# Kernel optimization log

Measured on AMD Instinct MI355X. Metric: run time of the kernel, lower is better.

Reference implementation:

```python
import jax, jax.numpy as jnp
import numpy as np

NUM_HEADS = 32
NUM_KV_HEADS = 8
HEAD_DIM = 128
HIDDEN = 4096
RANK = 8
ALPHA = 16.0
SCALING = ALPHA / RANK
EPS = 1e-8


def dora_linear(x, W, A, B, m):
    # DoRA: W_eff = W + scaling * B @ A; directional component normalized per
    # output row, rescaled by learned magnitude m.
    W_eff = W + SCALING * (B @ A)                      # [out, in]
    norm = jnp.linalg.norm(W_eff, axis=1)              # [out]
    W_d = W_eff * (m / (norm + EPS))[:, None]
    return x @ W_d.T


def setup_inputs() -> dict:
    key = jax.random.key(0)
    ks = jax.random.split(key, 16)
    B_, S = 2, 2048
    hidden_states = jax.random.normal(ks[0], (B_, S, HIDDEN), jnp.float32)
    # additive causal mask
    causal = jnp.triu(jnp.full((S, S), -1e9, jnp.float32), k=1)
    attention_mask = jnp.broadcast_to(causal, (B_, 1, S, S))

    def w(k, shape, scale=0.02):
        return scale * jax.random.normal(k, shape, jnp.float32)

    Wq = w(ks[1], (HIDDEN, HIDDEN)); Aq = w(ks[2], (RANK, HIDDEN)); Bq = w(ks[3], (HIDDEN, RANK))
    Wk = w(ks[4], (NUM_KV_HEADS * HEAD_DIM, HIDDEN)); Ak = w(ks[5], (RANK, HIDDEN)); Bk = w(ks[6], (NUM_KV_HEADS * HEAD_DIM, RANK))
    Wv = w(ks[7], (NUM_KV_HEADS * HEAD_DIM, HIDDEN)); Av = w(ks[8], (RANK, HIDDEN)); Bv = w(ks[9], (NUM_KV_HEADS * HEAD_DIM, RANK))
    Wo = w(ks[10], (HIDDEN, HIDDEN)); Ao = w(ks[11], (RANK, HIDDEN)); Bo = w(ks[12], (HIDDEN, RANK))
    # DoRA magnitude init: column-norm of base weight (per output row)
    mq = jnp.linalg.norm(Wq, axis=1)
    mk = jnp.linalg.norm(Wk, axis=1)
    mv = jnp.linalg.norm(Wv, axis=1)
    mo = jnp.linalg.norm(Wo, axis=1)
    return dict(hidden_states=hidden_states, attention_mask=attention_mask,
                Wq=Wq, Aq=Aq, Bq=Bq, mq=mq,
                Wk=Wk, Ak=Ak, Bk=Bk, mk=mk,
                Wv=Wv, Av=Av, Bv=Bv, mv=mv,
                Wo=Wo, Ao=Ao, Bo=Bo, mo=mo)


def reference(hidden_states, attention_mask,
              Wq, Aq, Bq, mq, Wk, Ak, Bk, mk,
              Wv, Av, Bv, mv, Wo, Ao, Bo, mo):
    bsz, q_len, _ = hidden_states.shape
    n_rep = NUM_HEADS // NUM_KV_HEADS

    q = dora_linear(hidden_states, Wq, Aq, Bq, mq)
    k = dora_linear(hidden_states, Wk, Ak, Bk, mk)
    v = dora_linear(hidden_states, Wv, Av, Bv, mv)

    q = q.reshape(bsz, q_len, NUM_HEADS, HEAD_DIM).transpose(0, 2, 1, 3)
    k = k.reshape(bsz, q_len, NUM_KV_HEADS, HEAD_DIM).transpose(0, 2, 1, 3)
    v = v.reshape(bsz, q_len, NUM_KV_HEADS, HEAD_DIM).transpose(0, 2, 1, 3)

    # _apply_rotary_pos_emb is a no-op in the source: (q, k) unchanged

    # repeat_kv for grouped-query attention
    k = jnp.repeat(k, n_rep, axis=1)  # [b, H, s, d]
    v = jnp.repeat(v, n_rep, axis=1)

    scale = 1.0 / jnp.sqrt(jnp.float32(HEAD_DIM))
    attn_weights = jnp.einsum('bhqd,bhkd->bhqk', q, k) * scale
    attn_weights = attn_weights + attention_mask
    attn_weights = jax.nn.softmax(attn_weights, axis=-1)
    attn_output = jnp.einsum('bhqk,bhkd->bhqd', attn_weights, v)
    attn_output = attn_output.transpose(0, 2, 1, 3).reshape(bsz, q_len, HIDDEN)
    attn_output = dora_linear(attn_output, Wo, Ao, Bo, mo)
    return attn_output
```

## Files before the change

kernel.cpp:

```cpp
#include <hip/hip_runtime.h>
#include <hip/hip_bf16.h>
#include <stdint.h>

#define HIDDEN 4096
#define RANK   8
#define SCALING 2.0f
#define EPS    1e-8f
#define SEQ    2048
#define BATCH  2
#define NH     32
#define NKVH   8
#define HD     128
#define MROWS  (BATCH*SEQ)
#define NQKV   6144

typedef __attribute__((ext_vector_type(8))) short bf16x8;
typedef __attribute__((ext_vector_type(4))) short bf16x4;
typedef __attribute__((ext_vector_type(4))) float f32x4;

__device__ __forceinline__ void gload_lds16(const void* g, void* lds) {
  __builtin_amdgcn_global_load_lds((__attribute__((address_space(1))) void*)g,
                                   (__attribute__((address_space(3))) void*)lds,
                                   16, 0, 0);
}

__device__ __forceinline__ unsigned short f2bf(float f) {
  __hip_bfloat16 h = __float2bfloat16(f);
  return *reinterpret_cast<unsigned short*>(&h);
}

__device__ __forceinline__ void store_c(float* p, float v) { *p = v; }
__device__ __forceinline__ void store_c(__hip_bfloat16* p, float v) { *p = __float2bfloat16(v); }

__device__ __forceinline__ bf16x8 lds_read8_b64(const short* p) {
  bf16x4 lo = *(const bf16x4*)p;
  bf16x4 hi = *(const bf16x4*)(p + 4);
  bf16x8 r;
  r[0]=lo[0]; r[1]=lo[1]; r[2]=lo[2]; r[3]=lo[3];
  r[4]=hi[0]; r[5]=hi[1]; r[6]=hi[2]; r[7]=hi[3];
  return r;
}

__device__ __forceinline__ void wd_row(const float* __restrict__ W, const float* __restrict__ A,
                                       const float* __restrict__ B, const float* __restrict__ m,
                                       unsigned short* __restrict__ out, int row, int tid,
                                       float* wsum) {
  float bl[RANK];
#pragma unroll
  for (int t = 0; t < RANK; ++t) bl[t] = SCALING * B[row*RANK + t];
  float ev[16];
  float ss = 0.f;
#pragma unroll
  for (int it = 0; it < 4; ++it) {
    const int j = it*1024 + tid*4;
    const float4 wv = *(const float4*)&W[(size_t)row*HIDDEN + j];
    float e0 = wv.x, e1 = wv.y, e2 = wv.z, e3 = wv.w;
#pragma unroll
    for (int t = 0; t < RANK; ++t) {
      const float4 av = *(const float4*)&A[t*HIDDEN + j];
      e0 += bl[t]*av.x; e1 += bl[t]*av.y; e2 += bl[t]*av.z; e3 += bl[t]*av.w;
    }
    ev[it*4+0]=e0; ev[it*4+1]=e1; ev[it*4+2]=e2; ev[it*4+3]=e3;
    ss += e0*e0 + e1*e1 + e2*e2 + e3*e3;
  }
#pragma unroll
  for (int off = 32; off > 0; off >>= 1) ss += __shfl_down(ss, off, 64);
  if ((tid & 63) == 0) wsum[tid >> 6] = ss;
  __syncthreads();
  const float norm = sqrtf(wsum[0]+wsum[1]+wsum[2]+wsum[3]);
  const float scl = m[row] / (norm + EPS);
#pragma unroll
  for (int it = 0; it < 4; ++it) {
    const int j = it*1024 + tid*4;
    ushort4 pk;
    pk.x = f2bf(ev[it*4+0]*scl); pk.y = f2bf(ev[it*4+1]*scl);
    pk.z = f2bf(ev[it*4+2]*scl); pk.w = f2bf(ev[it*4+3]*scl);
    *(ushort4*)&out[(size_t)row*HIDDEN + j] = pk;
  }
}

__launch_bounds__(256)
__global__ void prep_kernel(const float* __restrict__ x, unsigned short* __restrict__ xbf,
                            const float* Wq, const float* Aq, const float* Bq, const float* mq, unsigned short* wdq,
                            const float* Wk, const float* Ak, const float* Bk, const float* mk, unsigned short* wdk,
                            const float* Wv, const float* Av, const float* Bv, const float* mv, unsigned short* wdv,
                            const float* Wo, const float* Ao, const float* Bo, const float* mo, unsigned short* wdo) {
  __shared__ float wsum[4];
  const int bid = blockIdx.x;
  const int tid = threadIdx.x;
  if (bid < 16384) {
    const size_t i = ((size_t)bid * 256 + tid) * 4;
    const float4 v = *(const float4*)&x[i];
    ushort4 pk;
    pk.x = f2bf(v.x); pk.y = f2bf(v.y); pk.z = f2bf(v.z); pk.w = f2bf(v.w);
    *(ushort4*)&xbf[i] = pk;
  } else if (bid < 20480) {
    wd_row(Wq, Aq, Bq, mq, wdq, bid - 16384, tid, wsum);
  } else if (bid < 21504) {
    wd_row(Wk, Ak, Bk, mk, wdk, bid - 20480, tid, wsum);
  } else if (bid < 22528) {
    wd_row(Wv, Av, Bv, mv, wdv, bid - 21504, tid, wsum);
  } else {
    wd_row(Wo, Ao, Bo, mo, wdo, bid - 22528, tid, wsum);
  }
}

__launch_bounds__(256)
__global__ void wd_kernel(const float* __restrict__ W, const float* __restrict__ A,
                          const float* __restrict__ B, const float* __restrict__ m,
                          unsigned short* __restrict__ out) {
  __shared__ float wsum[4];
  wd_row(W, A, B, m, out, blockIdx.x, threadIdx.x, wsum);
}

template<typename CT>
__launch_bounds__(256)
__global__ void gemm_bt(const __hip_bfloat16* __restrict__ A,
                        const __hip_bfloat16* __restrict__ B,
                        CT* __restrict__ C, const int M, const int N, const int K) {
  __shared__ __hip_bfloat16 As[128*64];
  __shared__ __hip_bfloat16 Bs[128*64];
  const int tid = threadIdx.x;
  const int w = tid >> 6, l = tid & 63;
  const int tM = blockIdx.y * 128, tN = blockIdx.x * 128;
  const int wm = (w >> 1) * 64, wn = (w & 1) * 64;
  const int lr = l >> 3;
  const int lcs = ((l & 7) ^ lr) * 8;
  const int q4 = l >> 4;
  const int ln = l & 15;
  const int sw = ln & 7;
  f32x4 acc[4][4] = {};
  const __hip_bfloat16* Ab = A + (size_t)tM * K;
  const __hip_bfloat16* Bb = B + (size_t)tN * K;
  for (int k0 = 0; k0 < K; k0 += 64) {
    __syncthreads();
#pragma unroll
    for (int i = 0; i < 4; ++i) {
      const int rr = i*32 + w*8;
      gload_lds16(Ab + (size_t)(rr + lr)*K + (k0 + lcs), &As[rr*64]);
      gload_lds16(Bb + (size_t)(rr + lr)*K + (k0 + lcs), &Bs[rr*64]);
    }
    __syncthreads();
    const short* Ap = (const short*)As;
    const short* Bp = (const short*)Bs;
#pragma unroll
    for (int ks = 0; ks < 2; ++ks) {
      const int slot = ((ks*4 + q4) ^ sw) * 8;
      bf16x8 af[4], bff[4];
#pragma unroll
      for (int mi = 0; mi < 4; ++mi)
        af[mi] = *(const bf16x8*)&Ap[(wm + mi*16 + ln)*64 + slot];
#pragma unroll
      for (int ni = 0; ni < 4; ++ni)
        bff[ni] = *(const bf16x8*)&Bp[(wn + ni*16 + ln)*64 + slot];
#pragma unroll
      for (int mi = 0; mi < 4; ++mi)
#pragma unroll
        for (int ni = 0; ni < 4; ++ni)
          acc[mi][ni] = __builtin_amdgcn_mfma_f32_16x16x32_bf16(af[mi], bff[ni], acc[mi][ni], 0, 0, 0);
    }
  }
  const int r0 = tM + wm + q4*4;
  const int c0 = tN + wn + ln;
#pragma unroll
  for (int mi = 0; mi < 4; ++mi)
#pragma unroll
    for (int ni = 0; ni < 4; ++ni)
#pragma unroll
      for (int r = 0; r < 4; ++r)
        store_c(&C[(size_t)(r0 + mi*16 + r)*N + c0 + ni*16], acc[mi][ni][r]);
}

#define VT_S 68
#define PS_S 68
__launch_bounds__(256, 3)
__global__ void attn_kernel(const __hip_bfloat16* __restrict__ qkv,
                            __hip_bfloat16* __restrict__ out) {
  const int bid = blockIdx.x;
  const int qt = 15 - (bid >> 6);
  const int hb = bid & 63;
  const int h  = hb & 31;
  const int b  = hb >> 5;
  const int kvh = h >> 2;
  const int tid = threadIdx.x;
  const int w = tid >> 6, l = tid & 63;
  const int q4 = l >> 4;
  const int ln = l & 15;
  const int sw = ln & 7;

  __shared__ __hip_bfloat16 Ks[64*128];
  __shared__ __hip_bfloat16 Vt[128*VT_S];
  __shared__ __hip_bfloat16 Ps[4][2][16*PS_S];

  const __hip_bfloat16* kb = qkv + (size_t)(b*SEQ)*NQKV + HIDDEN + kvh*HD;
  const __hip_bfloat16* vb = qkv + (size_t)(b*SEQ)*NQKV + (HIDDEN+1024) + kvh*HD;

  const int Q0 = qt*128;

  const int krow = l >> 4;
  const int kchunk = ((l & 15) ^ krow ^ ((w & 1) << 2)) * 8;

  const int vc4 = (tid & 15) * 4;
  const int vd0 = (tid >> 4) * 8;

  bf16x8 aq[2][4];
#pragma unroll
  for (int hf = 0; hf < 2; ++hf) {
    const __hip_bfloat16* qr = qkv + (size_t)(b*SEQ + Q0 + hf*64 + w*16 + ln)*NQKV + h*HD;
#pragma unroll
    for (int ks = 0; ks < 4; ++ks) {
      uint4 raw = *(const uint4*)(qr + ks*32 + q4*8);
      aq[hf][ks] = *(const bf16x8*)&raw;
    }
  }

  f32x4 o[2][8] = {};
  float mx[2] = {-1e30f, -1e30f};
  float lsum[2] = {0.f, 0.f};
  const float sc = 0.08838834764831845f;
  const int qabs0 = Q0 + w*16 + ln;

  const int jmax = 2*qt + 1;
  for (int j = 0; j <= jmax; ++j) {
    const int do0 = (j <= 2*qt);
    __syncthreads();
#pragma unroll
    for (int i = 0; i < 4; ++i) {
      const int rr = i*16 + w*4;
      gload_lds16(kb + (size_t)(j*64 + rr + krow)*NQKV + kchunk, &Ks[rr*128]);
    }
    {
      uint4 r0 = *(const uint4*)(vb + (size_t)(j*64 + vc4 + 0)*NQKV + vd0);
      uint4 r1 = *(const uint4*)(vb + (size_t)(j*64 + vc4 + 1)*NQKV + vd0);
      uint4 r2 = *(const uint4*)(vb + (size_t)(j*64 + vc4 + 2)*NQKV + vd0);
      uint4 r3 = *(const uint4*)(vb + (size_t)(j*64 + vc4 + 3)*NQKV + vd0);
      const unsigned short* p0 = (const unsigned short*)&r0;
      const unsigned short* p1 = (const unsigned short*)&r1;
      const unsigned short* p2 = (const unsigned short*)&r2;
      const unsigned short* p3 = (const unsigned short*)&r3;
#pragma unroll
      for (int t = 0; t < 8; ++t) {
        ushort4 pk; pk.x = p0[t]; pk.y = p1[t]; pk.z = p2[t]; pk.w = p3[t];
        *(ushort4*)&Vt[(vd0 + t)*VT_S + vc4] = pk;
      }
    }
    __syncthreads();

    f32x4 s[2][4] = {};
    const short* Kp = (const short*)Ks;
#pragma unroll
    for (int ks = 0; ks < 4; ++ks) {
      const int slot = ((ks*4 + q4) ^ sw) * 8;
#pragma unroll
      for (int nt = 0; nt < 4; ++nt) {
        bf16x8 bk = *(const bf16x8*)&Kp[(nt*16 + ln)*128 + slot];
        if (do0) s[0][nt] = __builtin_amdgcn_mfma_f32_16x16x32_bf16(bk, aq[0][ks], s[0][nt], 0, 0, 0);
        s[1][nt] = __builtin_amdgcn_mfma_f32_16x16x32_bf16(bk, aq[1][ks], s[1][nt], 0, 0, 0);
      }
    }

#pragma unroll
    for (int hf = 0; hf < 2; ++hf) {
      if (hf == 0 && !do0) continue;
      const int qabs = qabs0 + hf*64;
      if (j == 2*qt + hf) {
#pragma unroll
        for (int nt = 0; nt < 4; ++nt)
#pragma unroll
          for (int r = 0; r < 4; ++r) {
            const int kvabs = j*64 + nt*16 + q4*4 + r;
            if (kvabs > qabs) s[hf][nt][r] = -1e30f;
          }
      }
      float vmax = mx[hf];
#pragma unroll
      for (int nt = 0; nt < 4; ++nt)
#pragma unroll
        for (int r = 0; r < 4; ++r) vmax = fmaxf(vmax, s[hf][nt][r]);
      vmax = fmaxf(vmax, __shfl_xor(vmax, 16, 64));
      vmax = fmaxf(vmax, __shfl_xor(vmax, 32, 64));
      const float alpha = __expf((mx[hf] - vmax) * sc);
      float rs = 0.f;
#pragma unroll
      for (int nt = 0; nt < 4; ++nt)
#pragma unroll
        for (int r = 0; r < 4; ++r) {
          const float e = __expf((s[hf][nt][r] - vmax) * sc);
          s[hf][nt][r] = e; rs += e;
        }
      rs += __shfl_xor(rs, 16, 64);
      rs += __shfl_xor(rs, 32, 64);
      mx[hf] = vmax;
      lsum[hf] = lsum[hf]*alpha + rs;
#pragma unroll
      for (int r = 0; r < 4; ++r) {
        const float ar = __shfl(alpha, q4*4 + r, 64);
#pragma unroll
        for (int ni = 0; ni < 8; ++ni) o[hf][ni][r] *= ar;
      }
      __hip_bfloat16* Pw = Ps[w][hf];
#pragma unroll
      for (int nt = 0; nt < 4; ++nt) {
        ushort4 pk;
        pk.x = f2bf(s[hf][nt][0]); pk.y = f2bf(s[hf][nt][1]);
        pk.z = f2bf(s[hf][nt][2]); pk.w = f2bf(s[hf][nt][3]);
        *(ushort4*)&Pw[ln*PS_S + nt*16 + q4*4] = pk;
      }
    }

    const short* Vp = (const short*)Vt;
    const short* Pp0 = (const short*)Ps[w][0];
    const short* Pp1 = (const short*)Ps[w][1];
#pragma unroll
    for (int ks = 0; ks < 2; ++ks) {
      bf16x8 ap0 = lds_read8_b64(&Pp0[ln*PS_S + ks*32 + q4*8]);
      bf16x8 ap1 = lds_read8_b64(&Pp1[ln*PS_S + ks*32 + q4*8]);
#pragma unroll
      for (int ni = 0; ni < 8; ++ni) {
        bf16x8 bv = lds_read8_b64(&Vp[(ni*16 + ln)*VT_S + ks*32 + q4*8]);
        if (do0) o[0][ni] = __builtin_amdgcn_mfma_f32_16x16x32_bf16(ap0, bv, o[0][ni], 0, 0, 0);
        o[1][ni] = __builtin_amdgcn_mfma_f32_16x16x32_bf16(ap1, bv, o[1][ni], 0, 0, 0);
      }
    }
  }

#pragma unroll
  for (int hf = 0; hf < 2; ++hf) {
    const int row0 = b*SEQ + Q0 + hf*64 + w*16 + q4*4;
#pragma unroll
    for (int r = 0; r < 4; ++r) {
      const float lr = __shfl(lsum[hf], q4*4 + r, 64);
      const float inv = 1.f / lr;
#pragma unroll
      for (int ni = 0; ni < 8; ++ni)
        out[(size_t)(row0 + r)*HIDDEN + h*HD + ni*16 + ln] = __float2bfloat16(o[hf][ni][r] * inv);
    }
  }
}

extern "C" void kernel_launch(void* const* d_in, const int* in_sizes, int n_in,
                              void* d_out, int out_size, void* d_ws, size_t ws_size,
                              hipStream_t stream) {
  (void)in_sizes; (void)n_in; (void)out_size;
  const float* x  = (const float*)d_in[0];
  const float* Wq = (const float*)d_in[2];
  const float* Aq = (const float*)d_in[3];
  const float* Bq = (const float*)d_in[4];
  const float* mq = (const float*)d_in[5];
  const float* Wk = (const float*)d_in[6];
  const float* Ak = (const float*)d_in[7];
  const float* Bk = (const float*)d_in[8];
  const float* mk = (const float*)d_in[9];
  const float* Wv = (const float*)d_in[10];
  const float* Av = (const float*)d_in[11];
  const float* Bv = (const float*)d_in[12];
  const float* mv = (const float*)d_in[13];
  const float* Wo = (const float*)d_in[14];
  const float* Ao = (const float*)d_in[15];
  const float* Bo = (const float*)d_in[16];
  const float* mo = (const float*)d_in[17];

  char* ws = (char*)d_ws;
  __hip_bfloat16* xbf = (__hip_bfloat16*)ws;
  __hip_bfloat16* wd  = (__hip_bfloat16*)(ws + (size_t)33554432);
  __hip_bfloat16* qkv = (__hip_bfloat16*)(ws + (size_t)83886080);
  const bool big = ws_size >= (size_t)167772160;
  __hip_bfloat16* wdo = big ? (__hip_bfloat16*)(ws + (size_t)134217728) : wd;

  prep_kernel<<<big ? 26624 : 22528, 256, 0, stream>>>(
      x, (unsigned short*)xbf,
      Wq, Aq, Bq, mq, (unsigned short*)wd,
      Wk, Ak, Bk, mk, (unsigned short*)(wd + (size_t)4096*4096),
      Wv, Av, Bv, mv, (unsigned short*)(wd + (size_t)5120*4096),
      Wo, Ao, Bo, mo, (unsigned short*)wdo);
  gemm_bt<__hip_bfloat16><<<dim3(48, 32), 256, 0, stream>>>(xbf, wd, qkv, MROWS, NQKV, HIDDEN);
  if (!big)
    wd_kernel<<<4096, 256, 0, stream>>>(Wo, Ao, Bo, mo, (unsigned short*)wdo);
  attn_kernel<<<1024, 256, 0, stream>>>(qkv, xbf);
  gemm_bt<float><<<dim3(32, 32), 256, 0, stream>>>(xbf, wdo, (float*)d_out, MROWS, HIDDEN, HIDDEN);
}
```

Baseline: 825.7 us.

## Replace GEMM with 256x256-tile double-buffered pipelined kernel and XCD-aware block mapping

Replaces the 128x128 single-buffered bf16 GEMM with a 512-thread kernel computing 256x256 tiles. The K loop is split into quarter-stages that issue the next stage's global-to-LDS loads while the current stage's MFMAs run, using a double-buffered 128KB LDS region, explicit vmcnt waits and s_setprio around the MFMA bursts. Block IDs are remapped so neighbouring tiles land on the same XCD for L2 reuse. The aim is to hide load latency and raise arithmetic intensity in both projection GEMMs. The cost is a heavier LDS and register footprint with lower occupancy, and correctness depends on the hand-placed barrier and waitcnt ordering.

```diff
diff --git a/kernel.cpp b/kernel.cpp
--- a/kernel.cpp
+++ b/kernel.cpp
@@ -113,62 +113,99 @@
   wd_row(W, A, B, m, out, blockIdx.x, threadIdx.x, wsum);
 }
 
+__device__ __forceinline__ void stage_unit(const __hip_bfloat16* __restrict__ Ab,
+                                           const __hip_bfloat16* __restrict__ Bb,
+                                           const int K, __hip_bfloat16* sbuf,
+                                           const int tau, const int j,
+                                           const int w, const int l, const int kchunk) {
+  const __hip_bfloat16* src = (j & 1) ? Bb : Ab;
+  __hip_bfloat16* dst = sbuf + ((tau & 1) << 15) + (j << 13);
+  const int k0 = (tau << 6) + ((j >> 1) << 5) + (kchunk << 3);
+  const int r0 = (w << 4) + (l >> 2);
+  gload_lds16(src + (size_t)r0 * K + k0, dst + (w << 9));
+  gload_lds16(src + (size_t)(r0 + 128) * K + k0, dst + 4096 + (w << 9));
+}
+
 template<typename CT>
-__launch_bounds__(256)
-__global__ void gemm_bt(const __hip_bfloat16* __restrict__ A,
+__launch_bounds__(512, 2)
+__global__ void gemm256(const __hip_bfloat16* __restrict__ A,
                         const __hip_bfloat16* __restrict__ B,
                         CT* __restrict__ C, const int M, const int N, const int K) {
-  __shared__ __hip_bfloat16 As[128*64];
-  __shared__ __hip_bfloat16 Bs[128*64];
+  (void)M;
+  __shared__ __hip_bfloat16 sb[65536];
   const int tid = threadIdx.x;
   const int w = tid >> 6, l = tid & 63;
-  const int tM = blockIdx.y * 128, tN = blockIdx.x * 128;
-  const int wm = (w >> 1) * 64, wn = (w & 1) * 64;
-  const int lr = l >> 3;
-  const int lcs = ((l & 7) ^ lr) * 8;
-  const int q4 = l >> 4;
-  const int ln = l & 15;
-  const int sw = ln & 7;
-  f32x4 acc[4][4] = {};
+  const int wr = w >> 2, wc = w & 3;
+  const int q4 = l >> 4, ln = l & 15;
+  const int nbn = N >> 8;
+  const int cpx = gridDim.x >> 3;
+  const int fid = (blockIdx.x & 7) * cpx + (blockIdx.x >> 3);
+  const int tM = (fid / nbn) << 8;
+  const int tN = (fid % nbn) << 8;
+  const int NT = K >> 6;
   const __hip_bfloat16* Ab = A + (size_t)tM * K;
   const __hip_bfloat16* Bb = B + (size_t)tN * K;
-  for (int k0 = 0; k0 < K; k0 += 64) {
-    __syncthreads();
-#pragma unroll
-    for (int i = 0; i < 4; ++i) {
-      const int rr = i*32 + w*8;
-      gload_lds16(Ab + (size_t)(rr + lr)*K + (k0 + lcs), &As[rr*64]);
-      gload_lds16(Bb + (size_t)(rr + lr)*K + (k0 + lcs), &Bs[rr*64]);
-    }
-    __syncthreads();
-    const short* Ap = (const short*)As;
-    const short* Bp = (const short*)Bs;
-#pragma unroll
-    for (int ks = 0; ks < 2; ++ks) {
-      const int slot = ((ks*4 + q4) ^ sw) * 8;
-      bf16x8 af[4], bff[4];
-#pragma unroll
-      for (int mi = 0; mi < 4; ++mi)
-        af[mi] = *(const bf16x8*)&Ap[(wm + mi*16 + ln)*64 + slot];
-#pragma unroll
-      for (int ni = 0; ni < 4; ++ni)
-        bff[ni] = *(const bf16x8*)&Bp[(wn + ni*16 + ln)*64 + slot];
-#pragma unroll
-      for (int mi = 0; mi < 4; ++mi)
+  const int kchunk = (l & 3) ^ ((l >> 3) & 3);
+  const int slotoff = (q4 ^ ((ln >> 1) & 3)) << 3;
+
+  f32x4 acc[8][4] = {};
+  bf16x8 bfr[4] = {};
+
+#pragma unroll
+  for (int s = 0; s < 6; ++s)
+    stage_unit(Ab, Bb, K, sb, s >> 2, s & 3, w, l, kchunk);
+  asm volatile("s_waitcnt vmcnt(4)" ::: "memory");
+  __builtin_amdgcn_s_barrier();
+
+  for (int t = 0; t < NT; ++t) {
+    const short* base = (const short*)sb + ((t & 1) << 15);
+#pragma unroll
+    for (int q = 0; q < 4; ++q) {
+      const int ks = q >> 1;
+      const int mh = q & 1;
+      bf16x8 af[4];
+      const short* Au = base + (ks << 14);
+#pragma unroll
+      for (int i = 0; i < 4; ++i) {
+        const int row = wr * 128 + (mh * 4 + i) * 16 + ln;
+        af[i] = *(const bf16x8*)&Au[row * 32 + slotoff];
+      }
+      if (mh == 0) {
+        const short* Bu = base + 8192 + (ks << 14);
+#pragma unroll
+        for (int i = 0; i < 4; ++i) {
+          const int row = wc * 64 + i * 16 + ln;
+          bfr[i] = *(const bf16x8*)&Bu[row * 32 + slotoff];
+        }
+      }
+      const int s = 4 * t + 6 + q;
+      if ((s >> 2) < NT)
+        stage_unit(Ab, Bb, K, sb, s >> 2, s & 3, w, l, kchunk);
+      __builtin_amdgcn_s_barrier();
+      __builtin_amdgcn_s_setprio(1);
+#pragma unroll
+      for (int i = 0; i < 4; ++i)
 #pragma unroll
         for (int ni = 0; ni < 4; ++ni)
-          acc[mi][ni] = __builtin_amdgcn_mfma_f32_16x16x32_bf16(af[mi], bff[ni], acc[mi][ni], 0, 0, 0);
-    }
-  }
-  const int r0 = tM + wm + q4*4;
-  const int c0 = tN + wn + ln;
-#pragma unroll
-  for (int mi = 0; mi < 4; ++mi)
+          acc[mh * 4 + i][ni] = __builtin_amdgcn_mfma_f32_16x16x32_bf16(af[i], bfr[ni], acc[mh * 4 + i][ni], 0, 0, 0);
+      __builtin_amdgcn_s_setprio(0);
+      if (q == 3 && t < NT - 1) {
+        if (t == NT - 2) asm volatile("s_waitcnt vmcnt(0)" ::: "memory");
+        else             asm volatile("s_waitcnt vmcnt(4)" ::: "memory");
+      }
+      __builtin_amdgcn_s_barrier();
+    }
+  }
+
+  const int r0 = tM + wr * 128 + q4 * 4;
+  const int c0 = tN + wc * 64 + ln;
+#pragma unroll
+  for (int mi = 0; mi < 8; ++mi)
 #pragma unroll
     for (int ni = 0; ni < 4; ++ni)
 #pragma unroll
       for (int r = 0; r < 4; ++r)
-        store_c(&C[(size_t)(r0 + mi*16 + r)*N + c0 + ni*16], acc[mi][ni][r]);
+        store_c(&C[(size_t)(r0 + mi * 16 + r) * N + c0 + ni * 16], acc[mi][ni][r]);
 }
 
 #define VT_S 68
@@ -373,9 +410,9 @@
       Wk, Ak, Bk, mk, (unsigned short*)(wd + (size_t)4096*4096),
       Wv, Av, Bv, mv, (unsigned short*)(wd + (size_t)5120*4096),
       Wo, Ao, Bo, mo, (unsigned short*)wdo);
-  gemm_bt<__hip_bfloat16><<<dim3(48, 32), 256, 0, stream>>>(xbf, wd, qkv, MROWS, NQKV, HIDDEN);
+  gemm256<__hip_bfloat16><<<384, 512, 0, stream>>>(xbf, wd, qkv, MROWS, NQKV, HIDDEN);
   if (!big)
     wd_kernel<<<4096, 256, 0, stream>>>(Wo, Ao, Bo, mo, (unsigned short*)wdo);
   attn_kernel<<<1024, 256, 0, stream>>>(qkv, xbf);
-  gemm_bt<float><<<dim3(32, 32), 256, 0, stream>>>(xbf, wdo, (float*)d_out, MROWS, HIDDEN, HIDDEN);
-}
+  gemm256<float><<<256, 512, 0, stream>>>(xbf, wdo, (float*)d_out, MROWS, HIDDEN, HIDDEN);
+}
```

After: 790.4 us. -4.3%, faster.
